# Performance work log

Hardware: AMD Instinct MI355X
Metric: run time of the kernel (lower is better)

Reference implementation:

```python
import jax, jax.numpy as jnp
import numpy as np

B, H, S, D = 2, 16, 2048, 64
MASK_P = 0.1  # sparse random mask; avoids all-heads-masked NaN under softmax(dim=1)


def setup_inputs() -> dict:
    key = jax.random.key(0)
    kq, kk, kv, km = jax.random.split(key, 4)
    Q = jax.random.normal(kq, (B, H, S, D), dtype=jnp.float32)
    K = jax.random.normal(kk, (B, H, S, D), dtype=jnp.float32)
    V = jax.random.normal(kv, (B, H, S, D), dtype=jnp.float32)
    mask_bool = jax.random.uniform(km, (B, H, S, S)) < MASK_P
    return {"Q": Q, "K": K, "V": V, "mask_bool": mask_bool, "head_dim": D}


def reference(Q, K, V, mask_bool, head_dim):
    scale = jnp.sqrt(jnp.asarray(head_dim, dtype=Q.dtype))
    # scores: [B, H, Sq, Sk]
    scores = jnp.einsum("bhqd,bhkd->bhqk", Q, K) / scale
    scores = jnp.where(mask_bool, -jnp.inf, scores)
    # NOTE: source uses torch.softmax(..., dim=1) -> normalize over HEADS axis.
    attention_weight = jax.nn.softmax(scores, axis=1)
    # dropout module treated as identity (eval mode)
    context = jnp.einsum("bhqk,bhkd->bhqd", attention_weight, V)
    # transpose(1, 2) -> [B, Sq, H, D]
    return jnp.transpose(context, (0, 2, 1, 3))
```

## Files before the change

kernel.cpp:

```cpp
#include <hip/hip_runtime.h>
#include <stdint.h>
#include <math.h>

#define BB 2
#define HH 16
#define SS 2048
#define DD 64
#define HSS ((size_t)SS * SS)
#define QE  ((size_t)BB * HH * SS * DD)
#define PME ((size_t)BB * SS * SS)

#define WPAD 72

typedef __attribute__((ext_vector_type(8))) short short8;
typedef __attribute__((ext_vector_type(4))) float float4v;

__device__ __forceinline__ float bflo(unsigned int u){ return __uint_as_float(u << 16); }
__device__ __forceinline__ float bfhi(unsigned int u){ return __uint_as_float(u & 0xffff0000u); }
__device__ __forceinline__ unsigned short f2bf(float f){
  unsigned int u = __float_as_uint(f);
  u += 0x7fffu + ((u >> 16) & 1u);
  return (unsigned short)(u >> 16);
}
__device__ __forceinline__ unsigned int pk2(float lo, float hi){
  return ((unsigned int)f2bf(hi) << 16) | (unsigned int)f2bf(lo);
}

__global__ void detect_mask_mode(const unsigned int* __restrict__ mw, int* __restrict__ mode_out){
  __shared__ int a32, af, a64;
  const int t = threadIdx.x;
  if (t == 0){ a32 = 1; af = 1; a64 = 1; }
  __syncthreads();
  int ok32 = 1, okf = 1, ok64 = 1;
  for (int idx = t; idx < 4096; idx += 256){
    const unsigned int w = mw[idx];
    if (w > 1u) ok32 = 0;
    if (w != 0u && w != 0x3F800000u) okf = 0;
    if ((idx & 1) ? (w != 0u) : (w > 1u)) ok64 = 0;
  }
  if (!ok32) atomicAnd(&a32, 0);
  if (!okf)  atomicAnd(&af, 0);
  if (!ok64) atomicAnd(&a64, 0);
  __syncthreads();
  if (t == 0){
    int mode;
    if (a64)      mode = 3;
    else if (a32) mode = 0;
    else if (af)  mode = 2;
    else          mode = 1;
    *mode_out = mode;
  }
}

__global__ __launch_bounds__(256) void pack_mask_kernel(
    const void* __restrict__ mask, const int* __restrict__ modep,
    unsigned short* __restrict__ pm)
{
  const int mode = *modep;
  const size_t tid  = (size_t)blockIdx.x * 256 + threadIdx.x;
  const size_t base = tid * 8;
  const size_t bq   = base >> 11;
  const int    k0   = (int)(base & (SS - 1));
  const size_t b    = bq >> 11;
  const size_t q    = bq & (SS - 1);

  unsigned short outv[8] = {0,0,0,0,0,0,0,0};

  if (mode == 0 || mode == 2){
    const unsigned int* p = (const unsigned int*)mask;
    #pragma unroll
    for (int h = 0; h < HH; ++h){
      const size_t e = ((b * HH + h) * SS + q) * SS + k0;
      const uint4 a = *(const uint4*)(p + e);
      const uint4 c = *(const uint4*)(p + e + 4);
      const unsigned short bit = (unsigned short)(1u << h);
      if (a.x) outv[0] |= bit;  if (a.y) outv[1] |= bit;
      if (a.z) outv[2] |= bit;  if (a.w) outv[3] |= bit;
      if (c.x) outv[4] |= bit;  if (c.y) outv[5] |= bit;
      if (c.z) outv[6] |= bit;  if (c.w) outv[7] |= bit;
    }
  } else if (mode == 1){
    const unsigned char* p = (const unsigned char*)mask;
    #pragma unroll
    for (int h = 0; h < HH; ++h){
      const size_t e = ((b * HH + h) * SS + q) * SS + k0;
      uint2 a = *(const uint2*)(p + e);
      const unsigned short bit = (unsigned short)(1u << h);
      #pragma unroll
      for (int j = 0; j < 4; ++j){
        if ((a.x >> (8*j)) & 0xffu) outv[j]     |= bit;
        if ((a.y >> (8*j)) & 0xffu) outv[4 + j] |= bit;
      }
    }
  } else {
    const unsigned int* p = (const unsigned int*)mask;
    #pragma unroll
    for (int h = 0; h < HH; ++h){
      const size_t e = (((b * HH + h) * SS + q) * SS + k0) * 2;
      const unsigned short bit = (unsigned short)(1u << h);
      #pragma unroll
      for (int j = 0; j < 4; ++j){
        const uint4 a = *(const uint4*)(p + e + j * 4);
        if (a.x) outv[j * 2]     |= bit;
        if (a.z) outv[j * 2 + 1] |= bit;
      }
    }
  }

  uint4 w;
  w.x = (unsigned int)outv[0] | ((unsigned int)outv[1] << 16);
  w.y = (unsigned int)outv[2] | ((unsigned int)outv[3] << 16);
  w.z = (unsigned int)outv[4] | ((unsigned int)outv[5] << 16);
  w.w = (unsigned int)outv[6] | ((unsigned int)outv[7] << 16);
  *(uint4*)(pm + base) = w;
}

__global__ void conv_bf16_kernel(const float* __restrict__ src, unsigned short* __restrict__ dst, float scale){
  const size_t i = ((size_t)blockIdx.x * 256 + threadIdx.x) * 8;
  const float4 a = *(const float4*)(src + i);
  const float4 b = *(const float4*)(src + i + 4);
  uint4 o;
  o.x = pk2(a.x * scale, a.y * scale);
  o.y = pk2(a.z * scale, a.w * scale);
  o.z = pk2(b.x * scale, b.y * scale);
  o.w = pk2(b.z * scale, b.w * scale);
  *(uint4*)(dst + i) = o;
}

__global__ void transp_v_kernel(const float* __restrict__ V, unsigned short* __restrict__ Vt){
  __shared__ unsigned short tile[64][66];
  const int t  = threadIdx.x;
  const int kt = blockIdx.x & 31;
  const int bh = blockIdx.x >> 5;
  {
    const int kr = t >> 2, dc = (t & 3) * 16;
    const float* src = V + ((size_t)bh * SS + (size_t)(kt * 64 + kr)) * DD + dc;
    #pragma unroll
    for (int c = 0; c < 4; ++c){
      const float4 v = *(const float4*)(src + c * 4);
      tile[kr][dc + c * 4 + 0] = f2bf(v.x);
      tile[kr][dc + c * 4 + 1] = f2bf(v.y);
      tile[kr][dc + c * 4 + 2] = f2bf(v.z);
      tile[kr][dc + c * 4 + 3] = f2bf(v.w);
    }
  }
  __syncthreads();
  {
    const int dr = t >> 2, kc = (t & 3) * 16;
    unsigned short* dst = Vt + ((size_t)bh * DD + dr) * SS + kt * 64 + kc;
    unsigned int w[8];
    #pragma unroll
    for (int p = 0; p < 8; ++p){
      w[p] = (unsigned int)tile[kc + 2*p][dr] | ((unsigned int)tile[kc + 2*p + 1][dr] << 16);
    }
    uint4 o0 = { w[0], w[1], w[2], w[3] };
    uint4 o1 = { w[4], w[5], w[6], w[7] };
    *(uint4*)(dst)     = o0;
    *(uint4*)(dst + 8) = o1;
  }
}

__global__ __launch_bounds__(256, 3) void attn_main_kernel(
    const unsigned short* __restrict__ Qb, const unsigned short* __restrict__ Kb,
    const unsigned short* __restrict__ Vt, const unsigned short* __restrict__ pm,
    float* __restrict__ out)
{
  __shared__ unsigned short W[HH * 16 * WPAD];

  const int t = threadIdx.x;
  const int wave = t >> 6, lane = t & 63, quad = lane >> 4, l16 = lane & 15;
  const int b = blockIdx.y, q0 = blockIdx.x * 16, kc = blockIdx.z;

  float4v O[4][4];
  #pragma unroll
  for (int i = 0; i < 4; ++i)
    #pragma unroll
    for (int j = 0; j < 4; ++j) O[i][j] = (float4v){0.f, 0.f, 0.f, 0.f};

  const unsigned short* qbase = Qb + ((size_t)(b * HH) * SS + (size_t)(q0 + l16)) * DD + quad * 8;

  #pragma unroll 1
  for (int ks = 0; ks < 16; ++ks){
    const int k0  = (kc * 16 + ks) * 64;
    const int k0w = k0 + wave * 16;

    const unsigned short* pmb = pm + ((size_t)b * SS + (size_t)(q0 + quad * 4)) * SS + (size_t)(k0w + l16);
    unsigned int m16[4];
    #pragma unroll
    for (int r = 0; r < 4; ++r) m16[r] = (unsigned int)pmb[(size_t)r * SS];

    unsigned int sp[HH][2];
    const unsigned short* kbase = Kb + ((size_t)(b * HH) * SS + (size_t)(k0w + l16)) * DD + quad * 8;

    #pragma unroll
    for (int h = 0; h < HH; ++h){
      const unsigned short* qp = qbase + (size_t)h * (SS * DD);
      const unsigned short* kp = kbase + (size_t)h * (SS * DD);
      const short8 a0 = *(const short8*)(qp);
      const short8 a1 = *(const short8*)(qp + 32);
      const short8 b0 = *(const short8*)(kp);
      const short8 b1 = *(const short8*)(kp + 32);
      float4v c = (float4v){0.f, 0.f, 0.f, 0.f};
      c = __builtin_amdgcn_mfma_f32_16x16x32_bf16(a0, b0, c, 0, 0, 0);
      c = __builtin_amdgcn_mfma_f32_16x16x32_bf16(a1, b1, c, 0, 0, 0);

      #pragma unroll
      for (int r = 0; r < 4; ++r) if ((m16[r] >> h) & 1u) c[r] = -INFINITY;

      sp[h][0] = pk2(c[0], c[1]);
      sp[h][1] = pk2(c[2], c[3]);
    }

    #pragma unroll
    for (int r = 0; r < 4; ++r){
      const int row = quad * 4 + r;
      float sv[HH];
      float m = -INFINITY;
      #pragma unroll
      for (int h = 0; h < HH; ++h){
        const unsigned int u = sp[h][r >> 1];
        const float f = (r & 1) ? bfhi(u) : bflo(u);
        sv[h] = f;
        m = fmaxf(m, f);
      }
      float sum = 0.f;
      #pragma unroll
      for (int h = 0; h < HH; ++h){
        const float e = (sv[h] != -INFINITY) ? __expf(sv[h] - m) : 0.f;
        sv[h] = e;
        sum += e;
      }
      const float rinv = (sum > 0.f) ? (1.0f / sum) : 0.f;
      const int col = wave * 16 + l16;
      #pragma unroll
      for (int h = 0; h < HH; ++h){
        W[h * (16 * WPAD) + row * WPAD + col] = f2bf(sv[h] * rinv);
      }
    }
    __syncthreads();

    #pragma unroll
    for (int hh = 0; hh < 4; ++hh){
      const int h = wave * 4 + hh;
      const unsigned short* vb = Vt + ((size_t)(b * HH + h) * DD + l16) * SS + k0 + quad * 8;
      #pragma unroll
      for (int kr = 0; kr < 2; ++kr){
        const short8 aw = *(const short8*)&W[h * (16 * WPAD) + l16 * WPAD + kr * 32 + quad * 8];
        #pragma unroll
        for (int dt = 0; dt < 4; ++dt){
          const short8 bv = *(const short8*)(vb + (size_t)dt * 16 * SS + kr * 32);
          O[hh][dt] = __builtin_amdgcn_mfma_f32_16x16x32_bf16(aw, bv, O[hh][dt], 0, 0, 0);
        }
      }
    }
    __syncthreads();
  }

  #pragma unroll
  for (int hh = 0; hh < 4; ++hh){
    const int h = wave * 4 + hh;
    #pragma unroll
    for (int dt = 0; dt < 4; ++dt){
      #pragma unroll
      for (int r = 0; r < 4; ++r){
        float* op = out + (((size_t)b * SS + (size_t)(q0 + quad * 4 + r)) * HH + h) * DD + dt * 16 + l16;
        unsafeAtomicAdd(op, O[hh][dt][r]);
      }
    }
  }
}

extern "C" void kernel_launch(void* const* d_in, const int* in_sizes, int n_in,
                              void* d_out, int out_size, void* d_ws, size_t ws_size,
                              hipStream_t stream)
{
  const float* Q = (const float*)d_in[0];
  const float* K = (const float*)d_in[1];
  const float* V = (const float*)d_in[2];
  const void* mask = d_in[3];

  uintptr_t base = (uintptr_t)d_ws;
  int* mode_ptr       = (int*)base;
  unsigned short* Qb  = (unsigned short*)(base + 64);
  unsigned short* Kb  = Qb + QE;
  unsigned short* Vt  = Kb + QE;
  unsigned short* pmp = Vt + QE;

  detect_mask_mode<<<1, 256, 0, stream>>>((const unsigned int*)mask, mode_ptr);
  pack_mask_kernel<<<(int)(PME / (256 * 8)), 256, 0, stream>>>(mask, mode_ptr, pmp);
  conv_bf16_kernel<<<2048, 256, 0, stream>>>(Q, Qb, 0.125f);
  conv_bf16_kernel<<<2048, 256, 0, stream>>>(K, Kb, 1.0f);
  transp_v_kernel<<<BB * HH * (SS / 64), 256, 0, stream>>>(V, Vt);
  hipMemsetAsync(d_out, 0, (size_t)out_size * sizeof(float), stream);

  dim3 grid(SS / 16, BB, 2);
  attn_main_kernel<<<grid, 256, 0, stream>>>(Qb, Kb, Vt, pmp, (float*)d_out);
}
```

Baseline: 1.169 ms.

## Stage Q in LDS, batch K loads, swizzle W, double-buffer V, remap grid

Q fragments for all 16 heads are loaded once per block into shared memory instead of being re-read from global memory on every key step. K loads are batched eight heads at a time so more loads are in flight before the score MFMAs. The W tile drops its padding in favour of an XOR swizzle to avoid LDS bank conflicts, and V fragments are double-buffered in registers across heads so loads overlap the MFMAs. The grid becomes a flat 1D launch with a custom block-index mapping, and launch bounds go from 3 to 2 blocks per CU, giving more registers per thread but lower occupancy.

```diff
diff --git a/kernel.cpp b/kernel.cpp
--- a/kernel.cpp
+++ b/kernel.cpp
@@ -6,11 +6,8 @@
 #define HH 16
 #define SS 2048
 #define DD 64
-#define HSS ((size_t)SS * SS)
 #define QE  ((size_t)BB * HH * SS * DD)
 #define PME ((size_t)BB * SS * SS)
-
-#define WPAD 72
 
 typedef __attribute__((ext_vector_type(8))) short short8;
 typedef __attribute__((ext_vector_type(4))) float float4v;
@@ -160,16 +157,21 @@
   }
 }
 
-__global__ __launch_bounds__(256, 3) void attn_main_kernel(
+__global__ __launch_bounds__(256, 2) void attn_main_kernel(
     const unsigned short* __restrict__ Qb, const unsigned short* __restrict__ Kb,
     const unsigned short* __restrict__ Vt, const unsigned short* __restrict__ pm,
     float* __restrict__ out)
 {
-  __shared__ unsigned short W[HH * 16 * WPAD];
+  __shared__ unsigned short Qf[HH * 2 * 512];
+  __shared__ unsigned short W[HH * 16 * 64];
 
   const int t = threadIdx.x;
   const int wave = t >> 6, lane = t & 63, quad = lane >> 4, l16 = lane & 15;
-  const int b = blockIdx.y, q0 = blockIdx.x * 16, kc = blockIdx.z;
+
+  const int L  = blockIdx.x;
+  const int b  = (L >> 1) & 1;
+  const int kc = (L >> 2) & 1;
+  const int q0 = (((L >> 3) << 1) | (L & 1)) * 16;
 
   float4v O[4][4];
   #pragma unroll
@@ -177,7 +179,16 @@
     #pragma unroll
     for (int j = 0; j < 4; ++j) O[i][j] = (float4v){0.f, 0.f, 0.f, 0.f};
 
-  const unsigned short* qbase = Qb + ((size_t)(b * HH) * SS + (size_t)(q0 + l16)) * DD + quad * 8;
+  #pragma unroll
+  for (int hh = 0; hh < 4; ++hh){
+    const int h = wave * 4 + hh;
+    const unsigned short* qp = Qb + ((size_t)(b * HH + h) * SS + (size_t)(q0 + l16)) * DD + quad * 8;
+    const short8 a0 = *(const short8*)(qp);
+    const short8 a1 = *(const short8*)(qp + 32);
+    *(short8*)&Qf[(h * 2 + 0) * 512 + lane * 8] = a0;
+    *(short8*)&Qf[(h * 2 + 1) * 512 + lane * 8] = a1;
+  }
+  __syncthreads();
 
   #pragma unroll 1
   for (int ks = 0; ks < 16; ++ks){
@@ -193,22 +204,27 @@
     const unsigned short* kbase = Kb + ((size_t)(b * HH) * SS + (size_t)(k0w + l16)) * DD + quad * 8;
 
     #pragma unroll
-    for (int h = 0; h < HH; ++h){
-      const unsigned short* qp = qbase + (size_t)h * (SS * DD);
-      const unsigned short* kp = kbase + (size_t)h * (SS * DD);
-      const short8 a0 = *(const short8*)(qp);
-      const short8 a1 = *(const short8*)(qp + 32);
-      const short8 b0 = *(const short8*)(kp);
-      const short8 b1 = *(const short8*)(kp + 32);
-      float4v c = (float4v){0.f, 0.f, 0.f, 0.f};
-      c = __builtin_amdgcn_mfma_f32_16x16x32_bf16(a0, b0, c, 0, 0, 0);
-      c = __builtin_amdgcn_mfma_f32_16x16x32_bf16(a1, b1, c, 0, 0, 0);
-
-      #pragma unroll
-      for (int r = 0; r < 4; ++r) if ((m16[r] >> h) & 1u) c[r] = -INFINITY;
-
-      sp[h][0] = pk2(c[0], c[1]);
-      sp[h][1] = pk2(c[2], c[3]);
+    for (int ch = 0; ch < 2; ++ch){
+      short8 kb0[8], kb1[8];
+      #pragma unroll
+      for (int j = 0; j < 8; ++j){
+        const unsigned short* kp = kbase + (size_t)(ch * 8 + j) * (SS * DD);
+        kb0[j] = *(const short8*)(kp);
+        kb1[j] = *(const short8*)(kp + 32);
+      }
+      #pragma unroll
+      for (int j = 0; j < 8; ++j){
+        const int h = ch * 8 + j;
+        const short8 a0 = *(const short8*)&Qf[(h * 2 + 0) * 512 + lane * 8];
+        const short8 a1 = *(const short8*)&Qf[(h * 2 + 1) * 512 + lane * 8];
+        float4v c = (float4v){0.f, 0.f, 0.f, 0.f};
+        c = __builtin_amdgcn_mfma_f32_16x16x32_bf16(a0, kb0[j], c, 0, 0, 0);
+        c = __builtin_amdgcn_mfma_f32_16x16x32_bf16(a1, kb1[j], c, 0, 0, 0);
+        #pragma unroll
+        for (int r = 0; r < 4; ++r) if ((m16[r] >> h) & 1u) c[r] = -INFINITY;
+        sp[h][0] = pk2(c[0], c[1]);
+        sp[h][1] = pk2(c[2], c[3]);
+      }
     }
 
     #pragma unroll
@@ -231,26 +247,49 @@
         sum += e;
       }
       const float rinv = (sum > 0.f) ? (1.0f / sum) : 0.f;
-      const int col = wave * 16 + l16;
+      const int col = (wave * 16 + l16) ^ ((row & 7) << 3);
       #pragma unroll
       for (int h = 0; h < HH; ++h){
-        W[h * (16 * WPAD) + row * WPAD + col] = f2bf(sv[h] * rinv);
+        W[h * 1024 + row * 64 + col] = f2bf(sv[h] * rinv);
       }
     }
     __syncthreads();
 
-    #pragma unroll
-    for (int hh = 0; hh < 4; ++hh){
-      const int h = wave * 4 + hh;
-      const unsigned short* vb = Vt + ((size_t)(b * HH + h) * DD + l16) * SS + k0 + quad * 8;
-      #pragma unroll
-      for (int kr = 0; kr < 2; ++kr){
-        const short8 aw = *(const short8*)&W[h * (16 * WPAD) + l16 * WPAD + kr * 32 + quad * 8];
+    {
+      short8 aw[8];
+      #pragma unroll
+      for (int hh = 0; hh < 4; ++hh)
         #pragma unroll
-        for (int dt = 0; dt < 4; ++dt){
-          const short8 bv = *(const short8*)(vb + (size_t)dt * 16 * SS + kr * 32);
-          O[hh][dt] = __builtin_amdgcn_mfma_f32_16x16x32_bf16(aw, bv, O[hh][dt], 0, 0, 0);
+        for (int kr = 0; kr < 2; ++kr){
+          const int h = wave * 4 + hh;
+          aw[hh * 2 + kr] = *(const short8*)&W[h * 1024 + l16 * 64 + ((kr * 32 + quad * 8) ^ ((l16 & 7) << 3))];
         }
+
+      short8 vb[2][8];
+      {
+        const unsigned short* v0 = Vt + ((size_t)(b * HH + wave * 4) * DD + l16) * SS + k0 + quad * 8;
+        #pragma unroll
+        for (int kr = 0; kr < 2; ++kr)
+          #pragma unroll
+          for (int dt = 0; dt < 4; ++dt)
+            vb[0][kr * 4 + dt] = *(const short8*)(v0 + (size_t)dt * 16 * SS + kr * 32);
+      }
+      #pragma unroll
+      for (int hh = 0; hh < 4; ++hh){
+        const int cur = hh & 1;
+        if (hh < 3){
+          const unsigned short* v1 = Vt + ((size_t)(b * HH + wave * 4 + hh + 1) * DD + l16) * SS + k0 + quad * 8;
+          #pragma unroll
+          for (int kr = 0; kr < 2; ++kr)
+            #pragma unroll
+            for (int dt = 0; dt < 4; ++dt)
+              vb[cur ^ 1][kr * 4 + dt] = *(const short8*)(v1 + (size_t)dt * 16 * SS + kr * 32);
+        }
+        #pragma unroll
+        for (int kr = 0; kr < 2; ++kr)
+          #pragma unroll
+          for (int dt = 0; dt < 4; ++dt)
+            O[hh][dt] = __builtin_amdgcn_mfma_f32_16x16x32_bf16(aw[hh * 2 + kr], vb[cur][kr * 4 + dt], O[hh][dt], 0, 0, 0);
       }
     }
     __syncthreads();
@@ -293,6 +332,5 @@
   transp_v_kernel<<<BB * HH * (SS / 64), 256, 0, stream>>>(V, Vt);
   hipMemsetAsync(d_out, 0, (size_t)out_size * sizeof(float), stream);
 
-  dim3 grid(SS / 16, BB, 2);
-  attn_main_kernel<<<grid, 256, 0, stream>>>(Qb, Kb, Vt, pmp, (float*)d_out);
-}
+  attn_main_kernel<<<512, 256, 0, stream>>>(Qb, Kb, Vt, pmp, (float*)d_out);
+}
```

New measurement: 1.003 ms. 1.16x faster.

## Restructure attention kernel to two-wave blocks with double-buffered packed head-pair weights

Applied to the files above, without the earlier changes.

Reworks the main attention kernel to use 128-thread blocks (two waves) over 32-key steps, with a 4-way key split and a 1D grid that places the key chunks of one query tile next to each other. Softmax weights are stored in LDS as packed bf16 head pairs in a double buffer, which removes the second barrier per iteration. Each wave now accumulates 8 heads, and the mask for the next step is prefetched. This raises the register count per thread, lowers threads per block, and doubles the number of atomic-add partial sums written to the output.

```diff
diff --git a/kernel.cpp b/kernel.cpp
--- a/kernel.cpp
+++ b/kernel.cpp
@@ -6,11 +6,10 @@
 #define HH 16
 #define SS 2048
 #define DD 64
-#define HSS ((size_t)SS * SS)
 #define QE  ((size_t)BB * HH * SS * DD)
 #define PME ((size_t)BB * SS * SS)
 
-#define WPAD 72
+#define WROW 36
 
 typedef __attribute__((ext_vector_type(8))) short short8;
 typedef __attribute__((ext_vector_type(4))) float float4v;
@@ -160,57 +159,75 @@
   }
 }
 
-__global__ __launch_bounds__(256, 3) void attn_main_kernel(
+__global__ __launch_bounds__(128, 2) void attn_main_kernel(
     const unsigned short* __restrict__ Qb, const unsigned short* __restrict__ Kb,
     const unsigned short* __restrict__ Vt, const unsigned short* __restrict__ pm,
     float* __restrict__ out)
 {
-  __shared__ unsigned short W[HH * 16 * WPAD];
+  __shared__ unsigned int Wp[2][8 * 16 * WROW];
 
   const int t = threadIdx.x;
   const int wave = t >> 6, lane = t & 63, quad = lane >> 4, l16 = lane & 15;
-  const int b = blockIdx.y, q0 = blockIdx.x * 16, kc = blockIdx.z;
-
-  float4v O[4][4];
+
+  const int L  = blockIdx.x;
+  const int kc = L & 3;
+  const int b  = (L >> 2) & 1;
+  const int q0 = (L >> 3) << 4;
+
+  float4v O[8][4];
   #pragma unroll
-  for (int i = 0; i < 4; ++i)
+  for (int i = 0; i < 8; ++i)
     #pragma unroll
     for (int j = 0; j < 4; ++j) O[i][j] = (float4v){0.f, 0.f, 0.f, 0.f};
 
   const unsigned short* qbase = Qb + ((size_t)(b * HH) * SS + (size_t)(q0 + l16)) * DD + quad * 8;
+  const unsigned short* kbas0 = Kb + ((size_t)(b * HH) * SS + (size_t)(kc * 512 + wave * 16 + l16)) * DD + quad * 8;
+  const unsigned short* pmrow = pm + ((size_t)b * SS + (size_t)(q0 + quad * 4)) * SS + (size_t)(kc * 512 + wave * 16 + l16);
+
+  unsigned int m16[4];
+  #pragma unroll
+  for (int r = 0; r < 4; ++r) m16[r] = (unsigned int)pmrow[(size_t)r * SS];
 
   #pragma unroll 1
   for (int ks = 0; ks < 16; ++ks){
-    const int k0  = (kc * 16 + ks) * 64;
-    const int k0w = k0 + wave * 16;
-
-    const unsigned short* pmb = pm + ((size_t)b * SS + (size_t)(q0 + quad * 4)) * SS + (size_t)(k0w + l16);
-    unsigned int m16[4];
-    #pragma unroll
-    for (int r = 0; r < 4; ++r) m16[r] = (unsigned int)pmb[(size_t)r * SS];
+    const int k0 = kc * 512 + ks * 32;
 
     unsigned int sp[HH][2];
-    const unsigned short* kbase = Kb + ((size_t)(b * HH) * SS + (size_t)(k0w + l16)) * DD + quad * 8;
-
-    #pragma unroll
-    for (int h = 0; h < HH; ++h){
-      const unsigned short* qp = qbase + (size_t)h * (SS * DD);
-      const unsigned short* kp = kbase + (size_t)h * (SS * DD);
-      const short8 a0 = *(const short8*)(qp);
-      const short8 a1 = *(const short8*)(qp + 32);
-      const short8 b0 = *(const short8*)(kp);
-      const short8 b1 = *(const short8*)(kp + 32);
-      float4v c = (float4v){0.f, 0.f, 0.f, 0.f};
-      c = __builtin_amdgcn_mfma_f32_16x16x32_bf16(a0, b0, c, 0, 0, 0);
-      c = __builtin_amdgcn_mfma_f32_16x16x32_bf16(a1, b1, c, 0, 0, 0);
-
-      #pragma unroll
-      for (int r = 0; r < 4; ++r) if ((m16[r] >> h) & 1u) c[r] = -INFINITY;
-
-      sp[h][0] = pk2(c[0], c[1]);
-      sp[h][1] = pk2(c[2], c[3]);
-    }
-
+    const unsigned short* kbase = kbas0 + (size_t)ks * 32 * DD;
+
+    #pragma unroll
+    for (int ch = 0; ch < 8; ++ch){
+      short8 qa0[2], qa1[2], kb0[2], kb1[2];
+      #pragma unroll
+      for (int j = 0; j < 2; ++j){
+        const int h = ch * 2 + j;
+        const unsigned short* qp = qbase + (size_t)h * (SS * DD);
+        const unsigned short* kp = kbase + (size_t)h * (SS * DD);
+        qa0[j] = *(const short8*)(qp);
+        qa1[j] = *(const short8*)(qp + 32);
+        kb0[j] = *(const short8*)(kp);
+        kb1[j] = *(const short8*)(kp + 32);
+      }
+      #pragma unroll
+      for (int j = 0; j < 2; ++j){
+        const int h = ch * 2 + j;
+        float4v c = (float4v){0.f, 0.f, 0.f, 0.f};
+        c = __builtin_amdgcn_mfma_f32_16x16x32_bf16(qa0[j], kb0[j], c, 0, 0, 0);
+        c = __builtin_amdgcn_mfma_f32_16x16x32_bf16(qa1[j], kb1[j], c, 0, 0, 0);
+        #pragma unroll
+        for (int r = 0; r < 4; ++r) if ((m16[r] >> h) & 1u) c[r] = -INFINITY;
+        sp[h][0] = pk2(c[0], c[1]);
+        sp[h][1] = pk2(c[2], c[3]);
+      }
+    }
+
+    if (ks < 15){
+      #pragma unroll
+      for (int r = 0; r < 4; ++r) m16[r] = (unsigned int)pmrow[(size_t)r * SS + (size_t)(ks + 1) * 32];
+    }
+
+    unsigned int* Wc = &Wp[ks & 1][0];
+    const int kdx = wave * 16 + l16;
     #pragma unroll
     for (int r = 0; r < 4; ++r){
       const int row = quad * 4 + r;
@@ -231,34 +248,48 @@
         sum += e;
       }
       const float rinv = (sum > 0.f) ? (1.0f / sum) : 0.f;
-      const int col = wave * 16 + l16;
-      #pragma unroll
-      for (int h = 0; h < HH; ++h){
-        W[h * (16 * WPAD) + row * WPAD + col] = f2bf(sv[h] * rinv);
+      #pragma unroll
+      for (int hp = 0; hp < 8; ++hp){
+        Wc[hp * (16 * WROW) + row * WROW + kdx] = pk2(sv[2 * hp] * rinv, sv[2 * hp + 1] * rinv);
       }
     }
     __syncthreads();
 
     #pragma unroll
-    for (int hh = 0; hh < 4; ++hh){
-      const int h = wave * 4 + hh;
-      const unsigned short* vb = Vt + ((size_t)(b * HH + h) * DD + l16) * SS + k0 + quad * 8;
-      #pragma unroll
-      for (int kr = 0; kr < 2; ++kr){
-        const short8 aw = *(const short8*)&W[h * (16 * WPAD) + l16 * WPAD + kr * 32 + quad * 8];
-        #pragma unroll
-        for (int dt = 0; dt < 4; ++dt){
-          const short8 bv = *(const short8*)(vb + (size_t)dt * 16 * SS + kr * 32);
-          O[hh][dt] = __builtin_amdgcn_mfma_f32_16x16x32_bf16(aw, bv, O[hh][dt], 0, 0, 0);
-        }
-      }
-    }
-    __syncthreads();
+    for (int hp2 = 0; hp2 < 4; ++hp2){
+      const int hp = wave * 4 + hp2;
+      const unsigned int* wb = &Wc[hp * (16 * WROW) + l16 * WROW + quad * 8];
+      const uint4 da = *(const uint4*)(wb);
+      const uint4 db = *(const uint4*)(wb + 4);
+      const unsigned int d0 = da.x, d1 = da.y, d2 = da.z, d3 = da.w;
+      const unsigned int d4 = db.x, d5 = db.y, d6 = db.z, d7 = db.w;
+      uint4 ue, uo;
+      ue.x = (d0 & 0xffffu) | (d1 << 16);
+      ue.y = (d2 & 0xffffu) | (d3 << 16);
+      ue.z = (d4 & 0xffffu) | (d5 << 16);
+      ue.w = (d6 & 0xffffu) | (d7 << 16);
+      uo.x = (d0 >> 16) | (d1 & 0xffff0000u);
+      uo.y = (d2 >> 16) | (d3 & 0xffff0000u);
+      uo.z = (d4 >> 16) | (d5 & 0xffff0000u);
+      uo.w = (d6 >> 16) | (d7 & 0xffff0000u);
+      const short8 ae = __builtin_bit_cast(short8, ue);
+      const short8 ao = __builtin_bit_cast(short8, uo);
+
+      const unsigned short* ve = Vt + ((size_t)(b * HH + 2 * hp) * DD + l16) * SS + k0 + quad * 8;
+      const unsigned short* vo = ve + (size_t)SS * DD;
+      #pragma unroll
+      for (int dt = 0; dt < 4; ++dt){
+        const short8 bve = *(const short8*)(ve + (size_t)dt * 16 * SS);
+        const short8 bvo = *(const short8*)(vo + (size_t)dt * 16 * SS);
+        O[hp2 * 2 + 0][dt] = __builtin_amdgcn_mfma_f32_16x16x32_bf16(ae, bve, O[hp2 * 2 + 0][dt], 0, 0, 0);
+        O[hp2 * 2 + 1][dt] = __builtin_amdgcn_mfma_f32_16x16x32_bf16(ao, bvo, O[hp2 * 2 + 1][dt], 0, 0, 0);
+      }
+    }
   }
 
   #pragma unroll
-  for (int hh = 0; hh < 4; ++hh){
-    const int h = wave * 4 + hh;
+  for (int hh = 0; hh < 8; ++hh){
+    const int h = wave * 8 + hh;
     #pragma unroll
     for (int dt = 0; dt < 4; ++dt){
       #pragma unroll
@@ -293,6 +324,5 @@
   transp_v_kernel<<<BB * HH * (SS / 64), 256, 0, stream>>>(V, Vt);
   hipMemsetAsync(d_out, 0, (size_t)out_size * sizeof(float), stream);
 
-  dim3 grid(SS / 16, BB, 2);
-  attn_main_kernel<<<grid, 256, 0, stream>>>(Qb, Kb, Vt, pmp, (float*)d_out);
-}
+  attn_main_kernel<<<1024, 128, 0, stream>>>(Qb, Kb, Vt, pmp, (float*)d_out);
+}
```

Result: faster. 1.124 ms (-3.8%).
